# Performance work log

Measured on AMD Instinct MI355X. Metric: run time of the kernel, lower is better.

Reference implementation:

```python
import jax, jax.numpy as jnp
import numpy as np

D, H_DIM, HEADS = 512, 2048, 8

def rmsnorm(x, w):
    eps = jnp.finfo(x.dtype).eps
    return x * jax.lax.rsqrt(jnp.mean(x * x, axis=-1, keepdims=True) + eps) * w

def setup_inputs() -> dict:
    key = jax.random.key(0)
    ks = jax.random.split(key, 16)
    B, N = 2, 2048
    s_d = 1.0 / np.sqrt(D)
    s_h = 1.0 / np.sqrt(H_DIM)
    inp = {
        "x": jax.random.normal(ks[0], (B, N, D), jnp.float32),
        "DA": jax.random.randint(ks[1], (B, 1, N, N), 0, 2, jnp.int32),
        "Wq": jax.random.normal(ks[2], (D, D), jnp.float32) * s_d,
        "bq": jnp.zeros((D,), jnp.float32),
        "Wk": jax.random.normal(ks[3], (D, D), jnp.float32) * s_d,
        "bk": jnp.zeros((D,), jnp.float32),
        "Wv": jax.random.normal(ks[4], (D, D), jnp.float32) * s_d,
        "bv": jnp.zeros((D,), jnp.float32),
        "W1": jax.random.normal(ks[5], (H_DIM, D), jnp.float32) * s_d,
        "b1": jnp.zeros((H_DIM,), jnp.float32),
        "W2": jax.random.normal(ks[6], (H_DIM, D), jnp.float32) * s_d,
        "b2": jnp.zeros((H_DIM,), jnp.float32),
        "W3": jax.random.normal(ks[7], (D, H_DIM), jnp.float32) * s_h,
        "b3": jnp.zeros((D,), jnp.float32),
        "g1": jnp.ones((D,), jnp.float32),
        "g2": jnp.ones((D,), jnp.float32),
    }
    return inp

def reference(x, DA, Wq, bq, Wk, bk, Wv, bv, W1, b1, W2, b2, W3, b3, g1, g2):
    B, N, _ = x.shape
    hd = D // HEADS  # head_dim = 64
    xn = rmsnorm(x, g1)
    # projections (torch Linear: y = x @ W.T + b), split heads -> [B,H,N,hd]
    def split(t):
        return t.reshape(B, N, HEADS, hd).transpose(0, 2, 1, 3)
    q = split(xn @ Wq.T + bq)
    k = split(xn @ Wk.T + bk)
    v = split(xn @ Wv.T + bv)
    scores = jnp.einsum("bhnd,bhmd->bhnm", q, k) / np.sqrt(hd)
    scores = jnp.where(DA == 0, jnp.asarray(-1e20, scores.dtype), scores)
    attn = jax.nn.softmax(scores, axis=-1)
    o = jnp.einsum("bhnm,bhmd->bhnd", attn, v)
    o = o.transpose(0, 2, 1, 3).reshape(B, N, D)
    h = x + o
    hn = rmsnorm(h, g2)
    x2 = hn @ W1.T + b1
    x3 = hn @ W2.T + b2
    out = h + (jax.nn.silu(x2) * x3) @ W3.T + b3
    return out
```

## Files before the change

kernel.cpp:

```cpp
#include <hip/hip_runtime.h>

typedef unsigned short u16;
typedef unsigned int   u32;
typedef unsigned long long u64;

using bf16x8 = __attribute__((ext_vector_type(8))) __bf16;
using f32x4  = __attribute__((ext_vector_type(4))) float;
using us8    = __attribute__((ext_vector_type(8))) u16;
using us4v   = __attribute__((ext_vector_type(4))) u16;
using u32x4  = __attribute__((ext_vector_type(4))) u32;

#define NB_TOK   4096
#define DD       512
#define HDIM     2048
#define SEQ      2048
#define EPS_F32  1.1920929e-7f
#define SM_SHIFT2 23.083120654223414f
#define Q_SCALE   0.18033688011112042f

__device__ __forceinline__ u16 f32_to_bf16(float f) {
  u32 u = __float_as_uint(f);
  u += 0x7fffu + ((u >> 16) & 1u);
  return (u16)(u >> 16);
}
__device__ __forceinline__ float bf16_to_f32(u16 h) {
  return __uint_as_float(((u32)h) << 16);
}
__device__ __forceinline__ bf16x8 ld_frag(const u16* p) {
  return __builtin_bit_cast(bf16x8, *(const us8*)p);
}
__device__ __forceinline__ void gload_lds16(const void* g, void* l) {
  __builtin_amdgcn_global_load_lds(
      (__attribute__((address_space(1))) void*)(void*)g,
      (__attribute__((address_space(3))) void*)l, 16, 0, 0);
}

__global__ __launch_bounds__(256) void k_pre(
    const float* __restrict__ wq, const float* __restrict__ wk,
    const float* __restrict__ wv, const float* __restrict__ w1,
    const float* __restrict__ w2, const float* __restrict__ w3,
    const int* __restrict__ da, const float* __restrict__ x,
    const float* __restrict__ g1,
    u16* __restrict__ wqkv, u16* __restrict__ w1b,
    u16* __restrict__ w2b, u16* __restrict__ w3b,
    u64* __restrict__ maskT, u16* __restrict__ xn) {
  int bx = blockIdx.x;
  if (bx < 3840) {
    int e = (bx * 256 + threadIdx.x) * 4;
    const float* src; u16* dst; int off;
    if      (e <  262144) { src = wq; dst = wqkv;          off = e; }
    else if (e <  524288) { src = wk; dst = wqkv + 262144; off = e -  262144; }
    else if (e <  786432) { src = wv; dst = wqkv + 524288; off = e -  524288; }
    else if (e < 1835008) { src = w1; dst = w1b;           off = e -  786432; }
    else if (e < 2883584) { src = w2; dst = w2b;           off = e - 1835008; }
    else                  { src = w3; dst = w3b;           off = e - 2883584; }
    float4 v = *(const float4*)(src + off);
    us4v o;
    o[0] = f32_to_bf16(v.x); o[1] = f32_to_bf16(v.y);
    o[2] = f32_to_bf16(v.z); o[3] = f32_to_bf16(v.w);
    *(us4v*)(dst + off) = o;
  } else if (bx < 4864) {
    int lane = threadIdx.x & 63, wave = threadIdx.x >> 6;
    int row = (bx - 3840) * 4 + wave;
    int b = row >> 11, r = row & 2047;
    const int* src = da + (size_t)row * SEQ;
    #pragma unroll 4
    for (int w = 0; w < 32; ++w) {
      int d = src[w * 64 + lane];
      u64 bal = __ballot(d != 0);
      if (lane == 0) maskT[((size_t)(b * 32 + w)) * SEQ + r] = bal;
    }
  } else {
    int lane = threadIdx.x & 63, wave = threadIdx.x >> 6;
    int row = (bx - 4864) * 4 + wave;
    size_t base = (size_t)row * DD + lane * 8;
    float4 a = *(const float4*)(x + base);
    float4 b = *(const float4*)(x + base + 4);
    float ss = a.x*a.x + a.y*a.y + a.z*a.z + a.w*a.w
             + b.x*b.x + b.y*b.y + b.z*b.z + b.w*b.w;
    #pragma unroll
    for (int m = 1; m < 64; m <<= 1) ss += __shfl_xor(ss, m);
    float sc = rsqrtf(ss * (1.0f / DD) + EPS_F32);
    float4 ga = *(const float4*)(g1 + lane * 8);
    float4 gb = *(const float4*)(g1 + lane * 8 + 4);
    us8 o;
    o[0] = f32_to_bf16(a.x * sc * ga.x); o[1] = f32_to_bf16(a.y * sc * ga.y);
    o[2] = f32_to_bf16(a.z * sc * ga.z); o[3] = f32_to_bf16(a.w * sc * ga.w);
    o[4] = f32_to_bf16(b.x * sc * gb.x); o[5] = f32_to_bf16(b.y * sc * gb.y);
    o[6] = f32_to_bf16(b.z * sc * gb.z); o[7] = f32_to_bf16(b.w * sc * gb.w);
    *(us8*)(xn + base) = o;
  }
}

template <int NB>
__device__ __forceinline__ void gemm32(const u16* __restrict__ A,
                                       const u16* __restrict__ B0,
                                       const u16* __restrict__ B1,
                                       int K, int mblk, int nblk,
                                       int kbeg, int iters,
                                       u16* lA, u16* lB,
                                       f32x4 (*acc)[4][2]) {
  const int lane = threadIdx.x & 63, wave = threadIdx.x >> 6;
  const int l15 = lane & 15, quad = lane >> 4;
  const int wmt = (wave >> 1) * 4, wnt = (wave & 1) * 2;
  constexpr int CPW = 2 + NB;

  auto stage = [&](int buf, int k0) {
    #pragma unroll
    for (int i = 0; i < CPW; ++i) {
      int id = wave * CPW + i;
      if (id < 8) {
        gload_lds16(A + (size_t)(mblk + id * 16 + l15) * K + k0 + quad * 8,
                    lA + buf * 4096 + id * 512);
      } else {
        int id2 = id - 8, bi = id2 >> 2, nt = id2 & 3;
        const u16* B = bi ? B1 : B0;
        gload_lds16(B + (size_t)(nblk + nt * 16 + l15) * K + k0 + quad * 8,
                    lB + bi * 4096 + buf * 2048 + nt * 512);
      }
    }
  };

  stage(0, kbeg);
  __syncthreads();
  for (int it = 0; it < iters; ++it) {
    if (it + 1 < iters) stage((it + 1) & 1, kbeg + (it + 1) * 32);
    int buf = it & 1;
    bf16x8 af[4];
    #pragma unroll
    for (int mt = 0; mt < 4; ++mt)
      af[mt] = ld_frag(lA + buf * 4096 + (wmt + mt) * 512 + lane * 8);
    #pragma unroll
    for (int bi = 0; bi < NB; ++bi)
      #pragma unroll
      for (int nt = 0; nt < 2; ++nt) {
        bf16x8 b = ld_frag(lB + bi * 4096 + buf * 2048 + (wnt + nt) * 512 + lane * 8);
        #pragma unroll
        for (int mt = 0; mt < 4; ++mt)
          acc[bi][mt][nt] = __builtin_amdgcn_mfma_f32_16x16x32_bf16(
              af[mt], b, acc[bi][mt][nt], 0, 0, 0);
      }
    __syncthreads();
  }
}

__global__ __launch_bounds__(256, 4) void k_qkv(const u16* __restrict__ xn,
                                                const u16* __restrict__ wqkv,
                                                const float* __restrict__ bq,
                                                const float* __restrict__ bk,
                                                const float* __restrict__ bv,
                                                u16* __restrict__ qb,
                                                u16* __restrict__ kb,
                                                u16* __restrict__ vt) {
  __shared__ u16 lA[8192], lB[4096];
  int z = blockIdx.z;
  const u16* Bp = wqkv + z * (DD * DD);
  const float* bias = (z == 0) ? bq : ((z == 1) ? bk : bv);
  float scale = (z == 0) ? Q_SCALE : 1.0f;
  int mblk = blockIdx.x * 128, nblk = blockIdx.y * 64;
  f32x4 acc[1][4][2];
  #pragma unroll
  for (int mt = 0; mt < 4; ++mt)
    #pragma unroll
    for (int nt = 0; nt < 2; ++nt) acc[0][mt][nt] = (f32x4)0.0f;
  gemm32<1>(xn, Bp, nullptr, DD, mblk, nblk, 0, 16, lA, lB, acc);
  int lane = threadIdx.x & 63, wave = threadIdx.x >> 6;
  int l15 = lane & 15, quad = lane >> 4;
  int wm = (wave >> 1) * 64, wn = (wave & 1) * 32;
  if (z < 2) {
    u16* out = z ? kb : qb;
    #pragma unroll
    for (int mt = 0; mt < 4; ++mt)
      #pragma unroll
      for (int nt = 0; nt < 2; ++nt) {
        int n = nblk + wn + nt * 16 + l15;
        float bn = bias[n];
        #pragma unroll
        for (int r = 0; r < 4; ++r) {
          int m = mblk + wm + mt * 16 + quad * 4 + r;
          out[(size_t)m * DD + n] = f32_to_bf16((acc[0][mt][nt][r] + bn) * scale);
        }
      }
  } else {
    #pragma unroll
    for (int mt = 0; mt < 4; ++mt)
      #pragma unroll
      for (int nt = 0; nt < 2; ++nt) {
        int n = nblk + wn + nt * 16 + l15;
        float bn = bias[n];
        int m = mblk + wm + mt * 16 + quad * 4;
        int b = m >> 11, tok = m & 2047;
        us4v o;
        #pragma unroll
        for (int r = 0; r < 4; ++r) o[r] = f32_to_bf16(acc[0][mt][nt][r] + bn);
        *(us4v*)(vt + ((size_t)(b * 8 + (n >> 6)) * 64 + (n & 63)) * SEQ + tok) = o;
      }
  }
}

__global__ __launch_bounds__(256, 4) void k_attn(const u16* __restrict__ q,
                                                 const u16* __restrict__ k,
                                                 const u16* __restrict__ vT,
                                                 const u64* __restrict__ maskT,
                                                 u16* __restrict__ Opart,
                                                 float* __restrict__ lpart) {
  __shared__ u16 lK[8192], lV[8192];
  int tid = threadIdx.x, lane = tid & 63, wave = tid >> 6;
  int l15 = lane & 15, quad = lane >> 4;
  int bh = blockIdx.y, b = bh >> 3, h = bh & 7;
  int q0 = blockIdx.x * 128;
  int z = blockIdx.z;
  int kvbase = z * 512;
  const u16* kg = k + (size_t)(b * SEQ + kvbase) * DD + h * 64;
  const u16* vg = vT + (size_t)bh * 64 * SEQ + kvbase;
  const u64* mg = maskT + ((size_t)(b * 32 + z * 8)) * SEQ + q0 + wave * 32 + l15;

  #pragma unroll
  for (int i = 0; i < 2; ++i) {
    int c = wave * 2 + i;
    int mt = c >> 1, ks = c & 1;
    gload_lds16(kg + (size_t)(mt * 16 + l15) * DD + ks * 32 + quad * 8, lK + c * 512);
    gload_lds16(vg + (size_t)(mt * 16 + l15) * SEQ + ks * 32 + quad * 8, lV + c * 512);
  }

  const u16* qrow = q + (size_t)(b * SEQ + q0 + wave * 32 + l15) * DD + h * 64;
  bf16x8 qa[2][2];
  #pragma unroll
  for (int nq = 0; nq < 2; ++nq)
    #pragma unroll
    for (int ks = 0; ks < 2; ++ks)
      qa[nq][ks] = ld_frag(qrow + (size_t)nq * 16 * DD + ks * 32 + quad * 8);
  __syncthreads();

  us8 ones_u;
  #pragma unroll
  for (int j = 0; j < 8; ++j) ones_u[j] = 0x3f80;
  const bf16x8 ones = __builtin_bit_cast(bf16x8, ones_u);

  const int idxA = (l15 + ((lane & 16) << 1)) * 4;
  const int idxB = idxA + 64;
  const bool hiTile = (quad & 2) != 0;

  f32x4 oa[2][4], oal[2];
  #pragma unroll
  for (int mq = 0; mq < 2; ++mq) {
    oal[mq] = (f32x4)0.0f;
    #pragma unroll
    for (int dt = 0; dt < 4; ++dt) oa[mq][dt] = (f32x4)0.0f;
  }

  u64 mw[2] = { mg[0], mg[16] };

  for (int t = 0; t < 8; ++t) {
    const u16* lKc = lK + (t & 1) * 4096;
    const u16* lVc = lV + (t & 1) * 4096;

    u64 mwn[2] = {0, 0};
    if (t + 1 < 8) {
      mwn[0] = mg[(size_t)(t + 1) * SEQ];
      mwn[1] = mg[(size_t)(t + 1) * SEQ + 16];
      int kv1 = (t + 1) * 64;
      u16* dK = lK + ((t + 1) & 1) * 4096;
      u16* dV = lV + ((t + 1) & 1) * 4096;
      #pragma unroll
      for (int i = 0; i < 2; ++i) {
        int c = wave * 2 + i;
        int mt = c >> 1, ks = c & 1;
        gload_lds16(kg + (size_t)(kv1 + mt * 16 + l15) * DD + ks * 32 + quad * 8, dK + c * 512);
        gload_lds16(vg + (size_t)(mt * 16 + l15) * SEQ + kv1 + ks * 32 + quad * 8, dV + c * 512);
      }
    }

    f32x4 sa[2][4];
    #pragma unroll
    for (int nq = 0; nq < 2; ++nq)
      #pragma unroll
      for (int mt = 0; mt < 4; ++mt) sa[nq][mt] = (f32x4)0.0f;
    #pragma unroll
    for (int ks = 0; ks < 2; ++ks) {
      bf16x8 ka[4];
      #pragma unroll
      for (int mt = 0; mt < 4; ++mt)
        ka[mt] = ld_frag(lKc + mt * 1024 + ks * 512 + lane * 8);
      #pragma unroll
      for (int nq = 0; nq < 2; ++nq)
        #pragma unroll
        for (int mt = 0; mt < 4; ++mt)
          sa[nq][mt] = __builtin_amdgcn_mfma_f32_16x16x32_bf16(
              ka[mt], qa[nq][ks], sa[nq][mt], 0, 0, 0);
    }

    u32 pk[2][4][2];
    #pragma unroll
    for (int nq = 0; nq < 2; ++nq) {
      u64 mq64 = mw[nq] >> (quad * 4);
      #pragma unroll
      for (int mt = 0; mt < 4; ++mt) {
        u32 nib = (u32)(mq64 >> (mt * 16)) & 0xFu;
        u32 pb[4];
        #pragma unroll
        for (int r = 0; r < 4; ++r) {
          float p = __builtin_amdgcn_exp2f(sa[nq][mt][r] - SM_SHIFT2);
          p = (nib >> r) & 1u ? p : 0.0f;
          pb[r] = __float_as_uint(p);
        }
        pk[nq][mt][0] = __builtin_amdgcn_perm(pb[1], pb[0], 0x07060302u);
        pk[nq][mt][1] = __builtin_amdgcn_perm(pb[3], pb[2], 0x07060302u);
      }
    }

    #pragma unroll
    for (int ks = 0; ks < 2; ++ks) {
      bf16x8 vb[4];
      #pragma unroll
      for (int dt = 0; dt < 4; ++dt)
        vb[dt] = ld_frag(lVc + dt * 1024 + ks * 512 + lane * 8);
      #pragma unroll
      for (int mq = 0; mq < 2; ++mq) {
        u32x4 regv;
        #pragma unroll
        for (int jr = 0; jr < 4; ++jr) {
          int idx = (jr < 2) ? idxA : idxB;
          int sel = jr & 1;
          u32 va = (u32)__builtin_amdgcn_ds_bpermute(idx, (int)pk[mq][2 * ks][sel]);
          u32 vbv = (u32)__builtin_amdgcn_ds_bpermute(idx, (int)pk[mq][2 * ks + 1][sel]);
          regv[jr] = hiTile ? vbv : va;
        }
        bf16x8 pa = __builtin_bit_cast(bf16x8, regv);
        #pragma unroll
        for (int dt = 0; dt < 4; ++dt)
          oa[mq][dt] = __builtin_amdgcn_mfma_f32_16x16x32_bf16(
              pa, vb[dt], oa[mq][dt], 0, 0, 0);
        oal[mq] = __builtin_amdgcn_mfma_f32_16x16x32_bf16(
            pa, ones, oal[mq], 0, 0, 0);
      }
    }

    mw[0] = mwn[0]; mw[1] = mwn[1];
    __syncthreads();
  }

  if (l15 == 0) {
    #pragma unroll
    for (int mq = 0; mq < 2; ++mq)
      #pragma unroll
      for (int r = 0; r < 4; ++r)
        lpart[((size_t)z * 16 + bh) * SEQ + q0 + wave * 32 + mq * 16 + quad * 4 + r] =
            oal[mq][r];
  }

  u16* Og = Opart + (size_t)z * NB_TOK * DD;
  #pragma unroll
  for (int mq = 0; mq < 2; ++mq)
    #pragma unroll
    for (int r = 0; r < 4; ++r) {
      int m = q0 + wave * 32 + mq * 16 + quad * 4 + r;
      u16* dst = Og + (size_t)(b * SEQ + m) * DD + h * 64;
      #pragma unroll
      for (int dt = 0; dt < 4; ++dt)
        dst[dt * 16 + l15] = f32_to_bf16(oa[mq][dt][r]);
    }
}

__global__ __launch_bounds__(256) void k_rms2(const float* __restrict__ x,
                                              const u16* __restrict__ Opart,
                                              const float* __restrict__ lpart,
                                              const float* __restrict__ b3,
                                              const float* __restrict__ g2,
                                              float* __restrict__ outinit,
                                              u16* __restrict__ hn) {
  int lane = threadIdx.x & 63, wave = threadIdx.x >> 6;
  int row = blockIdx.x * 4 + wave;
  int b = row >> 11, tok = row & 2047, hh = lane >> 3;
  size_t base = (size_t)row * DD + lane * 8;
  float lsum = 0.0f;
  #pragma unroll
  for (int z = 0; z < 4; ++z)
    lsum += lpart[((size_t)(z * 16 + b * 8 + hh)) * SEQ + tok];
  float inv = (lsum > 0.0f) ? (1.0f / lsum) : 0.0f;
  float ov[8] = {0,0,0,0,0,0,0,0};
  #pragma unroll
  for (int z = 0; z < 4; ++z) {
    us8 o = *(const us8*)(Opart + (size_t)z * NB_TOK * DD + base);
    #pragma unroll
    for (int j = 0; j < 8; ++j) ov[j] += bf16_to_f32(o[j]);
  }
  float4 a = *(const float4*)(x + base);
  float4 bb = *(const float4*)(x + base + 4);
  float hv[8];
  hv[0] = a.x  + ov[0] * inv; hv[1] = a.y  + ov[1] * inv;
  hv[2] = a.z  + ov[2] * inv; hv[3] = a.w  + ov[3] * inv;
  hv[4] = bb.x + ov[4] * inv; hv[5] = bb.y + ov[5] * inv;
  hv[6] = bb.z + ov[6] * inv; hv[7] = bb.w + ov[7] * inv;
  float ss = 0.0f;
  #pragma unroll
  for (int j = 0; j < 8; ++j) ss += hv[j] * hv[j];
  #pragma unroll
  for (int m = 1; m < 64; m <<= 1) ss += __shfl_xor(ss, m);
  float sc = rsqrtf(ss * (1.0f / DD) + EPS_F32);
  float4 c0 = *(const float4*)(b3 + lane * 8);
  float4 c1 = *(const float4*)(b3 + lane * 8 + 4);
  float4 w0 = {hv[0] + c0.x, hv[1] + c0.y, hv[2] + c0.z, hv[3] + c0.w};
  float4 w1 = {hv[4] + c1.x, hv[5] + c1.y, hv[6] + c1.z, hv[7] + c1.w};
  *(float4*)(outinit + base) = w0;
  *(float4*)(outinit + base + 4) = w1;
  float4 ga = *(const float4*)(g2 + lane * 8);
  float4 gb = *(const float4*)(g2 + lane * 8 + 4);
  us8 hb;
  hb[0] = f32_to_bf16(hv[0] * sc * ga.x); hb[1] = f32_to_bf16(hv[1] * sc * ga.y);
  hb[2] = f32_to_bf16(hv[2] * sc * ga.z); hb[3] = f32_to_bf16(hv[3] * sc * ga.w);
  hb[4] = f32_to_bf16(hv[4] * sc * gb.x); hb[5] = f32_to_bf16(hv[5] * sc * gb.y);
  hb[6] = f32_to_bf16(hv[6] * sc * gb.z); hb[7] = f32_to_bf16(hv[7] * sc * gb.w);
  *(us8*)(hn + base) = hb;
}

__global__ __launch_bounds__(256, 4) void k_ffn12(const u16* __restrict__ hn,
                                                  const u16* __restrict__ w1,
                                                  const u16* __restrict__ w2,
                                                  const float* __restrict__ b1,
                                                  const float* __restrict__ b2,
                                                  u16* __restrict__ g) {
  __shared__ u16 lA[8192], lB[8192];
  int mblk = blockIdx.x * 128, nblk = blockIdx.y * 64;
  f32x4 acc[2][4][2];
  #pragma unroll
  for (int bi = 0; bi < 2; ++bi)
    #pragma unroll
    for (int mt = 0; mt < 4; ++mt)
      #pragma unroll
      for (int nt = 0; nt < 2; ++nt) acc[bi][mt][nt] = (f32x4)0.0f;
  gemm32<2>(hn, w1, w2, DD, mblk, nblk, 0, 16, lA, lB, acc);
  int lane = threadIdx.x & 63, wave = threadIdx.x >> 6;
  int l15 = lane & 15, quad = lane >> 4;
  int wm = (wave >> 1) * 64, wn = (wave & 1) * 32;
  #pragma unroll
  for (int mt = 0; mt < 4; ++mt)
    #pragma unroll
    for (int nt = 0; nt < 2; ++nt) {
      int n = nblk + wn + nt * 16 + l15;
      float bb1 = b1[n], bb2 = b2[n];
      #pragma unroll
      for (int r = 0; r < 4; ++r) {
        int m = mblk + wm + mt * 16 + quad * 4 + r;
        float x2 = acc[0][mt][nt][r] + bb1;
        float x3 = acc[1][mt][nt][r] + bb2;
        float si = x2 / (1.0f + __expf(-x2));
        g[(size_t)m * HDIM + n] = f32_to_bf16(si * x3);
      }
    }
}

__global__ __launch_bounds__(256, 4) void k_ffn3(const u16* __restrict__ g,
                                                 const u16* __restrict__ w3,
                                                 float* __restrict__ out) {
  __shared__ u16 lA[8192], lB[4096];
  int mblk = blockIdx.x * 128, nblk = blockIdx.y * 64;
  f32x4 acc[1][4][2];
  #pragma unroll
  for (int mt = 0; mt < 4; ++mt)
    #pragma unroll
    for (int nt = 0; nt < 2; ++nt) acc[0][mt][nt] = (f32x4)0.0f;
  gemm32<1>(g, w3, nullptr, HDIM, mblk, nblk, 0, 64, lA, lB, acc);
  int lane = threadIdx.x & 63, wave = threadIdx.x >> 6;
  int l15 = lane & 15, quad = lane >> 4;
  int wm = (wave >> 1) * 64, wn = (wave & 1) * 32;
  #pragma unroll
  for (int mt = 0; mt < 4; ++mt)
    #pragma unroll
    for (int nt = 0; nt < 2; ++nt) {
      int n = nblk + wn + nt * 16 + l15;
      #pragma unroll
      for (int r = 0; r < 4; ++r) {
        int m = mblk + wm + mt * 16 + quad * 4 + r;
        size_t idx = (size_t)m * DD + n;
        out[idx] = out[idx] + acc[0][mt][nt][r];
      }
    }
}

#define MB(x) ((size_t)(x) * 1048576)
#define WS_XN    MB(0)
#define WS_WQKV  MB(4)
#define WS_W1B   MB(6)
#define WS_W2B   MB(8)
#define WS_W3B   MB(10)
#define WS_MASK  MB(12)
#define WS_QB    MB(16)
#define WS_KB    MB(20)
#define WS_VT    MB(24)
#define WS_OP    MB(28)
#define WS_LP    MB(44)
#define WS_HN    MB(45)
#define WS_G     MB(49)

extern "C" void kernel_launch(void* const* d_in, const int* in_sizes, int n_in,
                              void* d_out, int out_size, void* d_ws, size_t ws_size,
                              hipStream_t stream) {
  (void)in_sizes; (void)n_in; (void)out_size; (void)ws_size;
  const float* x  = (const float*)d_in[0];
  const int*   DA = (const int*)d_in[1];
  const float* Wq = (const float*)d_in[2];
  const float* bq = (const float*)d_in[3];
  const float* Wk = (const float*)d_in[4];
  const float* bk = (const float*)d_in[5];
  const float* Wv = (const float*)d_in[6];
  const float* bv = (const float*)d_in[7];
  const float* W1 = (const float*)d_in[8];
  const float* b1 = (const float*)d_in[9];
  const float* W2 = (const float*)d_in[10];
  const float* b2 = (const float*)d_in[11];
  const float* W3 = (const float*)d_in[12];
  const float* b3 = (const float*)d_in[13];
  const float* g1 = (const float*)d_in[14];
  const float* g2 = (const float*)d_in[15];
  float* out = (float*)d_out;
  char* w = (char*)d_ws;

  u16* xn   = (u16*)(w + WS_XN);
  u16* wqkv = (u16*)(w + WS_WQKV);
  u16* w1b  = (u16*)(w + WS_W1B);
  u16* w2b  = (u16*)(w + WS_W2B);
  u16* w3b  = (u16*)(w + WS_W3B);
  u64* mskT = (u64*)(w + WS_MASK);
  u16* qb   = (u16*)(w + WS_QB);
  u16* kb   = (u16*)(w + WS_KB);
  u16* vt   = (u16*)(w + WS_VT);
  u16* Op   = (u16*)(w + WS_OP);
  float* lp = (float*)(w + WS_LP);
  u16* hn   = (u16*)(w + WS_HN);
  u16* gb   = (u16*)(w + WS_G);

  k_pre<<<5888, 256, 0, stream>>>(Wq, Wk, Wv, W1, W2, W3, DA, x, g1,
                                  wqkv, w1b, w2b, w3b, mskT, xn);
  k_qkv<<<dim3(32, 8, 3), 256, 0, stream>>>(xn, wqkv, bq, bk, bv, qb, kb, vt);
  k_attn<<<dim3(16, 16, 4), 256, 0, stream>>>(qb, kb, vt, mskT, Op, lp);
  k_rms2<<<1024, 256, 0, stream>>>(x, Op, lp, b3, g2, out, hn);
  k_ffn12<<<dim3(32, 32), 256, 0, stream>>>(hn, w1b, w2b, b1, b2, gb);
  k_ffn3<<<dim3(32, 8), 256, 0, stream>>>(gb, w3b, out);
}
```

Baseline: 274.4 us.

## Read attention K/V fragments directly from global and split-K the final FFN GEMM

The attention kernel drops its double-buffered LDS staging of K and V and the per-tile barriers, loading MFMA fragments straight from global memory (relying on cache) instead. The last FFN GEMM is split along K into two halves written to scratch buffers, which doubles the grid from 256 blocks and adds a small merge kernel that sums both partials into the output. This trades LDS traffic and synchronisation for uncached-pattern global loads in attention, and extra memory traffic plus one launch for better occupancy in the FFN3 stage. The scratch buffers reuse the xn and q workspace regions, which are dead by that point.

```diff
diff --git a/kernel.cpp b/kernel.cpp
--- a/kernel.cpp
+++ b/kernel.cpp
@@ -204,24 +204,15 @@
                                                  const u64* __restrict__ maskT,
                                                  u16* __restrict__ Opart,
                                                  float* __restrict__ lpart) {
-  __shared__ u16 lK[8192], lV[8192];
   int tid = threadIdx.x, lane = tid & 63, wave = tid >> 6;
   int l15 = lane & 15, quad = lane >> 4;
   int bh = blockIdx.y, b = bh >> 3, h = bh & 7;
   int q0 = blockIdx.x * 128;
   int z = blockIdx.z;
   int kvbase = z * 512;
-  const u16* kg = k + (size_t)(b * SEQ + kvbase) * DD + h * 64;
-  const u16* vg = vT + (size_t)bh * 64 * SEQ + kvbase;
+  const u16* kg = k + (size_t)(b * SEQ + kvbase + l15) * DD + h * 64 + quad * 8;
+  const u16* vg = vT + (size_t)(bh * 64 + l15) * SEQ + kvbase + quad * 8;
   const u64* mg = maskT + ((size_t)(b * 32 + z * 8)) * SEQ + q0 + wave * 32 + l15;
-
-  #pragma unroll
-  for (int i = 0; i < 2; ++i) {
-    int c = wave * 2 + i;
-    int mt = c >> 1, ks = c & 1;
-    gload_lds16(kg + (size_t)(mt * 16 + l15) * DD + ks * 32 + quad * 8, lK + c * 512);
-    gload_lds16(vg + (size_t)(mt * 16 + l15) * SEQ + ks * 32 + quad * 8, lV + c * 512);
-  }
 
   const u16* qrow = q + (size_t)(b * SEQ + q0 + wave * 32 + l15) * DD + h * 64;
   bf16x8 qa[2][2];
@@ -230,7 +221,6 @@
     #pragma unroll
     for (int ks = 0; ks < 2; ++ks)
       qa[nq][ks] = ld_frag(qrow + (size_t)nq * 16 * DD + ks * 32 + quad * 8);
-  __syncthreads();
 
   us8 ones_u;
   #pragma unroll
@@ -252,23 +242,12 @@
   u64 mw[2] = { mg[0], mg[16] };
 
   for (int t = 0; t < 8; ++t) {
-    const u16* lKc = lK + (t & 1) * 4096;
-    const u16* lVc = lV + (t & 1) * 4096;
+    int kv0 = t * 64;
 
     u64 mwn[2] = {0, 0};
     if (t + 1 < 8) {
       mwn[0] = mg[(size_t)(t + 1) * SEQ];
       mwn[1] = mg[(size_t)(t + 1) * SEQ + 16];
-      int kv1 = (t + 1) * 64;
-      u16* dK = lK + ((t + 1) & 1) * 4096;
-      u16* dV = lV + ((t + 1) & 1) * 4096;
-      #pragma unroll
-      for (int i = 0; i < 2; ++i) {
-        int c = wave * 2 + i;
-        int mt = c >> 1, ks = c & 1;
-        gload_lds16(kg + (size_t)(kv1 + mt * 16 + l15) * DD + ks * 32 + quad * 8, dK + c * 512);
-        gload_lds16(vg + (size_t)(mt * 16 + l15) * SEQ + kv1 + ks * 32 + quad * 8, dV + c * 512);
-      }
     }
 
     f32x4 sa[2][4];
@@ -281,7 +260,7 @@
       bf16x8 ka[4];
       #pragma unroll
       for (int mt = 0; mt < 4; ++mt)
-        ka[mt] = ld_frag(lKc + mt * 1024 + ks * 512 + lane * 8);
+        ka[mt] = ld_frag(kg + (size_t)(kv0 + mt * 16) * DD + ks * 32);
       #pragma unroll
       for (int nq = 0; nq < 2; ++nq)
         #pragma unroll
@@ -314,7 +293,7 @@
       bf16x8 vb[4];
       #pragma unroll
       for (int dt = 0; dt < 4; ++dt)
-        vb[dt] = ld_frag(lVc + dt * 1024 + ks * 512 + lane * 8);
+        vb[dt] = ld_frag(vg + (size_t)(dt * 16) * SEQ + kv0 + ks * 32);
       #pragma unroll
       for (int mq = 0; mq < 2; ++mq) {
         u32x4 regv;
@@ -337,7 +316,6 @@
     }
 
     mw[0] = mwn[0]; mw[1] = mwn[1];
-    __syncthreads();
   }
 
   if (l15 == 0) {
@@ -452,15 +430,17 @@
 
 __global__ __launch_bounds__(256, 4) void k_ffn3(const u16* __restrict__ g,
                                                  const u16* __restrict__ w3,
-                                                 float* __restrict__ out) {
+                                                 float* __restrict__ p0,
+                                                 float* __restrict__ p1) {
   __shared__ u16 lA[8192], lB[4096];
-  int mblk = blockIdx.x * 128, nblk = blockIdx.y * 64;
+  int mblk = blockIdx.x * 128, nblk = blockIdx.y * 64, z = blockIdx.z;
   f32x4 acc[1][4][2];
   #pragma unroll
   for (int mt = 0; mt < 4; ++mt)
     #pragma unroll
     for (int nt = 0; nt < 2; ++nt) acc[0][mt][nt] = (f32x4)0.0f;
-  gemm32<1>(g, w3, nullptr, HDIM, mblk, nblk, 0, 64, lA, lB, acc);
+  gemm32<1>(g, w3, nullptr, HDIM, mblk, nblk, z * 1024, 32, lA, lB, acc);
+  float* dst = z ? p1 : p0;
   int lane = threadIdx.x & 63, wave = threadIdx.x >> 6;
   int l15 = lane & 15, quad = lane >> 4;
   int wm = (wave >> 1) * 64, wn = (wave & 1) * 32;
@@ -472,10 +452,21 @@
       #pragma unroll
       for (int r = 0; r < 4; ++r) {
         int m = mblk + wm + mt * 16 + quad * 4 + r;
-        size_t idx = (size_t)m * DD + n;
-        out[idx] = out[idx] + acc[0][mt][nt][r];
-      }
-    }
+        dst[(size_t)m * DD + n] = acc[0][mt][nt][r];
+      }
+    }
+}
+
+__global__ __launch_bounds__(256) void k_fmerge(const float* __restrict__ p0,
+                                                const float* __restrict__ p1,
+                                                float* __restrict__ out) {
+  int e = (blockIdx.x * 256 + threadIdx.x) * 4;
+  float4 a = *(const float4*)(p0 + e);
+  float4 b = *(const float4*)(p1 + e);
+  float4 o = *(const float4*)(out + e);
+  o.x += a.x + b.x; o.y += a.y + b.y;
+  o.z += a.z + b.z; o.w += a.w + b.w;
+  *(float4*)(out + e) = o;
 }
 
 #define MB(x) ((size_t)(x) * 1048576)
@@ -492,6 +483,8 @@
 #define WS_LP    MB(44)
 #define WS_HN    MB(45)
 #define WS_G     MB(49)
+#define WS_P0    MB(16)
+#define WS_P1    MB(0)
 
 extern "C" void kernel_launch(void* const* d_in, const int* in_sizes, int n_in,
                               void* d_out, int out_size, void* d_ws, size_t ws_size,
@@ -529,6 +522,8 @@
   float* lp = (float*)(w + WS_LP);
   u16* hn   = (u16*)(w + WS_HN);
   u16* gb   = (u16*)(w + WS_G);
+  float* p0 = (float*)(w + WS_P0);
+  float* p1 = (float*)(w + WS_P1);
 
   k_pre<<<5888, 256, 0, stream>>>(Wq, Wk, Wv, W1, W2, W3, DA, x, g1,
                                   wqkv, w1b, w2b, w3b, mskT, xn);
@@ -536,5 +531,6 @@
   k_attn<<<dim3(16, 16, 4), 256, 0, stream>>>(qb, kb, vt, mskT, Op, lp);
   k_rms2<<<1024, 256, 0, stream>>>(x, Op, lp, b3, g2, out, hn);
   k_ffn12<<<dim3(32, 32), 256, 0, stream>>>(hn, w1b, w2b, b1, b2, gb);
-  k_ffn3<<<dim3(32, 8), 256, 0, stream>>>(gb, w3b, out);
-}
+  k_ffn3<<<dim3(32, 8, 2), 256, 0, stream>>>(gb, w3b, p0, p1);
+  k_fmerge<<<2048, 256, 0, stream>>>(p0, p1, out);
+}
```

Result: slower. 319.4 us (+16.4%).
